# Kernel optimization log

Measured on AMD Instinct MI355X. Metric: run time of the kernel, lower is better.

Reference implementation:

```python
import jax, jax.numpy as jnp
import numpy as np

NUM_HEADS = 16


def _rel_shift(x):
    # x: [b, n, i, L]  (Transformer-XL relative shift trick)
    b, n, i, L = x.shape
    xt = jnp.transpose(x, (2, 3, 0, 1))              # [i, L, b, n]
    zero = jnp.zeros((i, 1, b, n), xt.dtype)
    xp = jnp.concatenate([zero, xt], axis=1)         # [i, L+1, b, n]
    xp = xp.reshape(L + 1, i, b, n)
    xt = xp[1:].reshape(i, L, b, n)
    return jnp.transpose(xt, (2, 3, 0, 1))


def _forward(x, bias, pos_emb, pos_bias_u, pos_bias_v, cache, indice_bool,
             sent_weights, Wq, bq, Wk, bk, Wv, bv, Wo, bo, Wr, br):
    B, I, H = x.shape
    nh = NUM_HEADS
    D = H // nh
    aff = lambda t, W, b: t @ W.T + b
    sh = lambda t: jnp.transpose(t.reshape(B, -1, nh, D), (0, 2, 1, 3))

    q, k, v = aff(x, Wq, bq), aff(x, Wk, bk), aff(x, Wv, bv)
    r = aff(jnp.swapaxes(pos_emb, 0, 1), Wr, br)
    qh, kh, vh, rh = sh(q), sh(k), sh(v), sh(r)

    N, cB, L, _ = cache.shape
    clen = N * L
    cflat = jnp.swapaxes(cache, 0, 1).reshape(cB, clen, H)
    ckh = jnp.transpose(sh(aff(cflat, Wk, bk)).reshape(cB, nh, N, L, D), (2, 0, 1, 3, 4))  # [N,B,nh,L,D]
    cvh = jnp.transpose(sh(aff(cflat, Wv, bv)).reshape(cB, nh, N, L, D), (2, 0, 1, 3, 4))
    cache_rh = jnp.transpose(rh[:, :, :clen].reshape(B, nh, N, L, D), (2, 0, 1, 3, 4))
    rh = rh[:, :, clen:]

    qh = qh * D ** -0.5
    quh = qh + pos_bias_u[:, None, :]
    qvh = qh + pos_bias_v[:, None, :]

    AC = jnp.einsum('bnid,bnjd->bnij', quh, kh) + bias
    BD = jnp.einsum('bnid,bnjd->bnij', qvh, rh)

    pre_AC = jnp.einsum('bnid,ibk->kbnid', quh, indice_bool)
    cAC = jnp.einsum('kbnid,kbnld->kbnil', pre_AC, ckh)
    cAC = jnp.transpose(cAC, (1, 2, 3, 0, 4)).reshape(B, nh, I, clen)
    AC = jnp.concatenate([cAC, AC], axis=-1)

    pre_BD = jnp.einsum('bnid,ibk->kbnid', qvh, indice_bool)
    cBD = jnp.einsum('kbnid,kbnld->kbnil', pre_BD, cache_rh)
    cBD = jnp.transpose(cBD, (1, 2, 3, 0, 4)).reshape(B, nh, I, clen)
    BD = jnp.concatenate([cBD, BD], axis=-1)

    logits = AC + _rel_shift(BD)
    w = jax.nn.softmax(logits, axis=-1)
    cw, w = w[..., :clen], w[..., clen:]

    cw = jnp.transpose(cw.reshape(B, nh, I, N, L), (3, 0, 1, 2, 4))  # [N,b,nh,i,L]
    cw = jnp.einsum('kbnij,ibk->bnikj', cw, sent_weights).reshape(B, nh, I, clen)
    cvh2 = jnp.transpose(cvh, (1, 2, 0, 3, 4)).reshape(B, nh, clen, D)

    out = (jnp.einsum('bnij,bnjd->bnid', w, vh)
           + jnp.einsum('bnij,bnjd->bnid', cw, cvh2))
    out = jnp.transpose(out, (0, 2, 1, 3)).reshape(B, I, H)
    return aff(out, Wo, bo)


def setup_inputs() -> dict:
    key = jax.random.key(0)
    ks = jax.random.split(key, 12)
    B, I, H, N, L = 4, 512, 1024, 4, 512
    R = N * L + I
    D = H // NUM_HEADS
    s = H ** -0.5
    return {
        'x': jax.random.normal(ks[0], (B, I, H), jnp.float32),
        'bias': jnp.zeros((1, 1, I, I), jnp.float32),
        'pos_emb': jax.random.normal(ks[1], (R, B, H), jnp.float32),
        'pos_bias_u': jax.random.normal(ks[2], (NUM_HEADS, D), jnp.float32),
        'pos_bias_v': jax.random.normal(ks[3], (NUM_HEADS, D), jnp.float32),
        'cache': jax.random.normal(ks[4], (N, B, L, H), jnp.float32),
        'indice_bool': jnp.ones((I, B, N), jnp.float32),
        'sent_weights': jax.random.uniform(ks[5], (I, B, N), jnp.float32),
        'Wq': jax.random.normal(ks[6], (H, H), jnp.float32) * s,
        'bq': jnp.zeros((H,), jnp.float32),
        'Wk': jax.random.normal(ks[7], (H, H), jnp.float32) * s,
        'bk': jnp.zeros((H,), jnp.float32),
        'Wv': jax.random.normal(ks[8], (H, H), jnp.float32) * s,
        'bv': jnp.zeros((H,), jnp.float32),
        'Wo': jax.random.normal(ks[9], (H, H), jnp.float32) * s,
        'bo': jnp.zeros((H,), jnp.float32),
        'Wr': jax.random.normal(ks[10], (H, H), jnp.float32) * s,
        'br': jnp.zeros((H,), jnp.float32),
    }


def reference(x, bias, pos_emb, pos_bias_u, pos_bias_v, cache, indice_bool,
              sent_weights, Wq, bq, Wk, bk, Wv, bv, Wo, bo, Wr, br):
    return _forward(x, bias, pos_emb, pos_bias_u, pos_bias_v, cache,
                    indice_bool, sent_weights, Wq, bq, Wk, bk, Wv, bv,
                    Wo, bo, Wr, br)
```

## Files before the change

kernel.cpp:

```cpp
#include <hip/hip_runtime.h>
#include <hip/hip_bf16.h>


typedef __hip_bfloat16 hbf16;
typedef __attribute__((ext_vector_type(8))) short short8;
typedef __attribute__((ext_vector_type(4))) short short4v;
typedef __attribute__((ext_vector_type(4))) float f32x4;

typedef __attribute__((address_space(1))) const unsigned int as1c_uint;
typedef __attribute__((address_space(3))) unsigned int as3_uint;

#define DEV static __device__ __forceinline__

DEV void gl_lds16(const void* g, void* l) {
  __builtin_amdgcn_global_load_lds((as1c_uint*)g, (as3_uint*)l, 16, 0, 0);
}

DEV short bf_bits(float f) {
  hbf16 h = __float2bfloat16(f);
  return __builtin_bit_cast(short, h);
}

DEV f32x4 mfma16(short8 a, short8 b, f32x4 c) {
  return __builtin_amdgcn_mfma_f32_16x16x32_bf16(a, b, c, 0, 0, 0);
}

__global__ __launch_bounds__(256) void pack_all(
    const float* __restrict__ x, const float* __restrict__ cache,
    const float* __restrict__ pe, const float* __restrict__ Wq,
    const float* __restrict__ Wk, const float* __restrict__ Wv,
    const float* __restrict__ Wo, const float* __restrict__ Wr,
    short* __restrict__ x_bf, short* __restrict__ cf_bf,
    short* __restrict__ pe_bf, short* __restrict__ wq_bf,
    short* __restrict__ wk_bf, short* __restrict__ wv_bf,
    short* __restrict__ wo_bf, short* __restrict__ wr_bf) {
  const int bid = blockIdx.x, tid = threadIdx.x;
  const float* src;
  short* dst;
  size_t sidx, didx;
  if (bid < 2048) {
    int c = bid * 256 + tid;
    src = x; dst = x_bf; sidx = c; didx = c;
  } else if (bid < 10240) {
    int c = (bid - 2048) * 256 + tid;
    int h4 = c & 255, m = c >> 8;
    int b = m >> 11, j = m & 2047;
    size_t srow = ((size_t)(j >> 9) * 4 + b) * 512 + (j & 511);
    src = cache; dst = cf_bf; sidx = srow * 256 + h4; didx = c;
  } else if (bid < 20480) {
    int c = (bid - 10240) * 256 + tid;
    int h4 = c & 255, m = c >> 8;
    int b = m / 2560, j = m - b * 2560;
    size_t srow = (size_t)j * 4 + b;
    src = pe; dst = pe_bf; sidx = srow * 256 + h4; didx = c;
  } else {
    int e = bid - 20480;
    int w = e >> 10;
    int c = (e & 1023) * 256 + tid;
    switch (w) {
      case 0: src = Wq; dst = wq_bf; break;
      case 1: src = Wk; dst = wk_bf; break;
      case 2: src = Wv; dst = wv_bf; break;
      case 3: src = Wo; dst = wo_bf; break;
      default: src = Wr; dst = wr_bf; break;
    }
    sidx = c; didx = c;
  }
  float4 v = ((const float4*)src)[sidx];
  short4v s; s.x = bf_bits(v.x); s.y = bf_bits(v.y); s.z = bf_bits(v.z); s.w = bf_bits(v.w);
  ((short4v*)dst)[didx] = s;
}

#define GEMM_KLOOP(Asrc, Wsrc)                                                  \
  f32x4 acc[4][4];                                                              \
  _Pragma("unroll") for (int a_ = 0; a_ < 4; a_++)                              \
  _Pragma("unroll") for (int b_ = 0; b_ < 4; b_++)                              \
      acc[a_][b_] = (f32x4){0.f, 0.f, 0.f, 0.f};                                \
  for (int k0 = 0; k0 < 1024; k0 += 32) {                                       \
    _Pragma("unroll") for (int q = 0; q < 2; q++) {                             \
      const int ci = (wid * 2 + q) * 64 + lane;                                 \
      const int r = ci >> 2, cc = (ci & 3) << 3;                                \
      gl_lds16(Asrc + (size_t)(m0 + r) * 1024 + k0 + cc,                        \
               (char*)As + (wid * 2 + q) * 1024);                               \
      gl_lds16(Wsrc + (size_t)(n0 + r) * 1024 + k0 + cc,                        \
               (char*)Bs + (wid * 2 + q) * 1024);                               \
    }                                                                           \
    __syncthreads();                                                            \
    short8 af[4], bfv[4];                                                       \
    _Pragma("unroll") for (int mi = 0; mi < 4; mi++)                            \
        af[mi] = *(const short8*)(As + (wm * 64 + mi * 16 + lr) * 32 + lk * 8); \
    _Pragma("unroll") for (int ni = 0; ni < 4; ni++)                            \
        bfv[ni] = *(const short8*)(Bs + (wn * 64 + ni * 16 + lr) * 32 + lk * 8);\
    _Pragma("unroll") for (int mi = 0; mi < 4; mi++)                            \
    _Pragma("unroll") for (int ni = 0; ni < 4; ni++)                            \
        acc[mi][ni] = mfma16(af[mi], bfv[ni], acc[mi][ni]);                     \
    __syncthreads();                                                            \
  }

__global__ __launch_bounds__(256) void gemm_kv(
    const short* __restrict__ A, const short* __restrict__ W,
    const float* __restrict__ bk, const float* __restrict__ bv,
    short* __restrict__ KF, short* __restrict__ VT) {
  __shared__ short As[128 * 32], Bs[128 * 32];
  const int tid = threadIdx.x, wid = tid >> 6, lane = tid & 63;
  const int lr = lane & 15, lk = lane >> 4;
  const int wm = wid >> 1, wn = wid & 1;
  const int flat = blockIdx.y * 16 + blockIdx.x;
  const int xcd = flat & 7, kk = flat >> 3;
  const int nt = kk & 15, mt = xcd * 10 + (kk >> 4);
  const int m0 = mt * 128, n0 = nt * 128;

  GEMM_KLOOP(A, W)

#pragma unroll
  for (int mi = 0; mi < 4; mi++) {
    const int mrow = m0 + wm * 64 + mi * 16 + lk * 4;
#pragma unroll
    for (int ni = 0; ni < 4; ni++) {
      const int col = n0 + wn * 64 + ni * 16 + lr;
      const float bc = (col < 1024) ? bk[col] : bv[col - 1024];
#pragma unroll
      for (int r = 0; r < 4; r++) {
        const int m = mrow + r;
        const float v = acc[mi][ni][r] + bc;
        int bb, jj;
        if (m < 8192) { bb = m >> 11; jj = m & 2047; }
        else { int mm = m - 8192; bb = mm >> 9; jj = 2048 + (mm & 511); }
        if (col < 1024) {
          const int n = col >> 6, d = col & 63;
          KF[((size_t)(bb * 16 + n) * 2560 + jj) * 64 + d] = bf_bits(v);
        } else {
          const int cv = col - 1024, n = cv >> 6, d = cv & 63;
          VT[((size_t)(bb * 16 + n) * 64 + d) * 2560 + jj] = bf_bits(v);
        }
      }
    }
  }
}

__global__ __launch_bounds__(256) void gemm_qr(
    const short* __restrict__ pe_bf, const short* __restrict__ x_bf,
    const short* __restrict__ Wr, const short* __restrict__ Wq,
    const float* __restrict__ br, const float* __restrict__ bq,
    const float* __restrict__ pu, const float* __restrict__ pv,
    short* __restrict__ RF, short* __restrict__ QU, short* __restrict__ QV) {
  __shared__ short As[128 * 32], Bs[128 * 32];
  const int tid = threadIdx.x, wid = tid >> 6, lane = tid & 63;
  const int lr = lane & 15, lk = lane >> 4;
  const int wm = wid >> 1, wn = wid & 1;
  const int flat = blockIdx.y * 8 + blockIdx.x;
  const int xcd = flat & 7, kk = flat >> 3;
  const int nt = kk & 7, mt = xcd * 12 + (kk >> 3);
  const bool isQ = (mt >= 80);
  const short* Asrc = isQ ? x_bf : pe_bf;
  const short* Wsrc = isQ ? Wq : Wr;
  const int m0 = (isQ ? mt - 80 : mt) * 128, n0 = nt * 128;

  GEMM_KLOOP(Asrc, Wsrc)

#pragma unroll
  for (int mi = 0; mi < 4; mi++) {
    const int mrow = m0 + wm * 64 + mi * 16 + lk * 4;
#pragma unroll
    for (int ni = 0; ni < 4; ni++) {
      const int col = n0 + wn * 64 + ni * 16 + lr;
      const float bc = isQ ? bq[col] : br[col];
      const int n = col >> 6, d = col & 63;
#pragma unroll
      for (int r = 0; r < 4; r++) {
        const int m = mrow + r;
        const float v = acc[mi][ni][r] + bc;
        if (isQ) {
          const int b = m >> 9, i = m & 511;
          const float qs = v * 0.125f;
          const size_t o = ((size_t)(b * 16 + n) * 512 + i) * 64 + d;
          QU[o] = bf_bits(qs + pu[col]);
          QV[o] = bf_bits(qs + pv[col]);
        } else {
          const int b = m / 2560, j = m - b * 2560;
          RF[((size_t)(b * 16 + n) * 2560 + j) * 64 + d] = bf_bits(v);
        }
      }
    }
  }
}

__global__ __launch_bounds__(256) void gemm_out(
    const short* __restrict__ A, const short* __restrict__ W,
    const float* __restrict__ bias, float* __restrict__ of) {
  __shared__ short As[128 * 32], Bs[128 * 32];
  const int tid = threadIdx.x, wid = tid >> 6, lane = tid & 63;
  const int lr = lane & 15, lk = lane >> 4;
  const int wm = wid >> 1, wn = wid & 1;
  const int flat = blockIdx.y * 8 + blockIdx.x;
  const int xcd = flat & 7, kk = flat >> 3;
  const int nt = kk & 7, mt = xcd * 2 + (kk >> 3);
  const int m0 = mt * 128, n0 = nt * 128;

  GEMM_KLOOP(A, W)

#pragma unroll
  for (int mi = 0; mi < 4; mi++) {
    const int mrow = m0 + wm * 64 + mi * 16 + lk * 4;
#pragma unroll
    for (int ni = 0; ni < 4; ni++) {
      const int col = n0 + wn * 64 + ni * 16 + lr;
      const float bc = bias[col];
#pragma unroll
      for (int r = 0; r < 4; r++)
        of[(size_t)(mrow + r) * 1024 + col] = acc[mi][ni][r] + bc;
    }
  }
}

__global__ __launch_bounds__(256, 2) void fused_attn(
    const short* __restrict__ QU, const short* __restrict__ QV,
    const short* __restrict__ KF, const short* __restrict__ RF,
    const short* __restrict__ VT, const float* __restrict__ ib,
    const float* __restrict__ sw, const float* __restrict__ bias,
    short* __restrict__ attn) {
  __shared__ short Ks[2][64 * 64];
  __shared__ short Rs[2][128 * 64];
  __shared__ float PsU[4][16 * 84];
  __shared__ float ibs[65 * 4];
  __shared__ float sws[64 * 4];

  const int tid = threadIdx.x, wid = tid >> 6, lane = tid & 63;
  const int p = blockIdx.x, it = blockIdx.y;
  const int b = p >> 4, hn = p & 15;
  const int I0 = it * 64, iw = wid * 16;
  const int lr = lane & 15, lg4 = lane >> 4;
  float* Psw = PsU[wid];
  short* Ptw = (short*)Psw;

  for (int t5 = tid; t5 < 260; t5 += 256) {
    int r = t5 >> 2, k = t5 & 3;
    int gi = I0 + r; if (gi > 511) gi = 511;
    ibs[t5] = ib[gi * 16 + b * 4 + k];
  }
  {
    int r = tid >> 2, k = tid & 3;
    sws[tid] = sw[(I0 + r) * 16 + b * 4 + k];
  }

  short8 qu[2], qv[2], qvp[2];
  {
    const short* QUb = QU + ((size_t)p * 512 + I0) * 64;
    const short* QVb = QV + ((size_t)p * 512 + I0) * 64;
    int rowp = I0 + iw + lr + 1; if (rowp > 511) rowp = 511;
    const short* QVn = QV + ((size_t)p * 512 + rowp) * 64;
#pragma unroll
    for (int s = 0; s < 2; s++) {
      qu[s]  = *(const short8*)(QUb + (iw + lr) * 64 + s * 32 + lg4 * 8);
      qv[s]  = *(const short8*)(QVb + (iw + lr) * 64 + s * 32 + lg4 * 8);
      qvp[s] = *(const short8*)(QVn + s * 32 + lg4 * 8);
    }
  }
  const short* KFp = KF + (size_t)p * 2560 * 64;
  const short* RFp = RF + (size_t)p * 2560 * 64;
  const short* VTp = VT + (size_t)p * 64 * 2560;

  auto stageK = [&](int j0, int buf) {
#pragma unroll
    for (int q = 0; q < 2; q++) {
      int e = wid * 2 + q;
      int row = e * 8 + (lane >> 3);
      int ch = (lane & 7) ^ (row & 7);
      gl_lds16(KFp + (size_t)(j0 + row) * 64 + ch * 8,
               (char*)Ks + buf * 8192 + e * 1024);
    }
  };
  auto stageR = [&](int band, int buf) {
#pragma unroll
    for (int q = 0; q < 4; q++) {
      int e = wid * 4 + q;
      int row = e * 8 + (lane >> 3);
      int rg = band + row; rg = rg < 0 ? 0 : (rg > 2559 ? 2559 : rg);
      int ch = (lane & 7) ^ (row & 7);
      gl_lds16(RFp + (size_t)rg * 64 + ch * 8,
               (char*)Rs + buf * 16384 + e * 1024);
    }
  };
  auto bfragK = [&](int buf, int row, int s) -> short8 {
    return *(const short8*)((const char*)Ks + buf * 8192 + row * 128 +
                            (((s * 4 + lg4) ^ (row & 7)) << 4));
  };
  auto bfragR = [&](int buf, int row, int s) -> short8 {
    return *(const short8*)((const char*)Rs + buf * 16384 + row * 128 +
                            (((s * 4 + lg4) ^ (row & 7)) << 4));
  };
  auto bd_lds = [&](short8 a0, short8 a1, int ro, int band, int buf) {
#pragma unroll
    for (int ctl = 0; ctl < 5; ctl++) {
      int cidx = (3 - wid) * 16 + ctl * 16 + lr;
      f32x4 acc = (f32x4){0.f, 0.f, 0.f, 0.f};
      acc = mfma16(a0, bfragR(buf, cidx, 0), acc);
      acc = mfma16(a1, bfragR(buf, cidx, 1), acc);
      int scol = band + cidx;
#pragma unroll
      for (int r = 0; r < 4; r++) {
        int ii = lg4 * 4 + r;
        float v = acc[r];
        if ((unsigned)scol < 2048u) v *= ibs[(iw + ii + ro) * 4 + (scol >> 9)];
        Psw[ii * 84 + ctl * 16 + lr] = v;
      }
    }
  };
  auto bd_glb = [&](short8 a0, short8 a1, int ro, int band) {
#pragma unroll
    for (int ctl = 0; ctl < 5; ctl++) {
      int cidx = (3 - wid) * 16 + ctl * 16 + lr;
      int rg = band + cidx; rg = rg < 0 ? 0 : (rg > 2559 ? 2559 : rg);
      const short* rb = RFp + (size_t)rg * 64 + lg4 * 8;
      short8 b0 = *(const short8*)(rb);
      short8 b1 = *(const short8*)(rb + 32);
      f32x4 acc = (f32x4){0.f, 0.f, 0.f, 0.f};
      acc = mfma16(a0, b0, acc);
      acc = mfma16(a1, b1, acc);
      int scol = band + cidx;
#pragma unroll
      for (int r = 0; r < 4; r++) {
        int ii = lg4 * 4 + r;
        float v = acc[r];
        if ((unsigned)scol < 2048u) v *= ibs[(iw + ii + ro) * 4 + (scol >> 9)];
        Psw[ii * 84 + ctl * 16 + lr] = v;
      }
    }
  };

  float m_[4], l_[4];
  f32x4 o[4];
#pragma unroll
  for (int r = 0; r < 4; r++) { m_[r] = -1e30f; l_[r] = 0.f; }
#pragma unroll
  for (int dt = 0; dt < 4; dt++) o[dt] = (f32x4){0.f, 0.f, 0.f, 0.f};

  {
    const int tb0 = 448 - I0;
    stageK(0, 0);
    stageR((tb0 <= 2559) ? tb0 : tb0 - 2561, 0);
  }
  __syncthreads();
  int cur = 0;

  for (int j0 = 0; j0 < 2560; j0 += 64) {
    const int tb = j0 + 448 - I0;
    const bool ph1 = (tb <= 2559);
    const bool strad = ph1 && (tb >= 2435);

    if (j0 + 64 < 2560) {
      const int tbn = tb + 64;
      stageK(j0 + 64, cur ^ 1);
      stageR((tbn <= 2559) ? tbn : tbn - 2561, cur ^ 1);
    }

    short8 vf0[4], vf1[4];
#pragma unroll
    for (int q = 0; q < 4; q++) {
      const short* vb = VTp + (size_t)(q * 16 + lr) * 2560 + j0 + lg4 * 8;
      vf0[q] = *(const short8*)(vb);
      vf1[q] = *(const short8*)(vb + 32);
    }

    f32x4 lgt[4];
#pragma unroll
    for (int jt = 0; jt < 4; jt++) {
      f32x4 acc = (f32x4){0.f, 0.f, 0.f, 0.f};
      acc = mfma16(qu[0], bfragK(cur, jt * 16 + lr, 0), acc);
      acc = mfma16(qu[1], bfragK(cur, jt * 16 + lr, 1), acc);
      lgt[jt] = acc;
    }
    if (j0 < 2048) {
      float s0[4];
#pragma unroll
      for (int r = 0; r < 4; r++) s0[r] = ibs[(iw + lg4 * 4 + r) * 4 + (j0 >> 9)];
#pragma unroll
      for (int jt = 0; jt < 4; jt++)
#pragma unroll
        for (int r = 0; r < 4; r++) lgt[jt][r] *= s0[r];
    } else {
#pragma unroll
      for (int jt = 0; jt < 4; jt++)
#pragma unroll
        for (int r = 0; r < 4; r++) {
          int i = I0 + iw + lg4 * 4 + r;
          lgt[jt][r] += bias[(size_t)i * 512 + (j0 - 2048) + jt * 16 + lr];
        }
    }

    if (ph1) bd_lds(qv[0], qv[1], 0, tb, cur);
    else     bd_lds(qvp[0], qvp[1], 1, tb - 2561, cur);
#pragma unroll
    for (int jt = 0; jt < 4; jt++)
#pragma unroll
      for (int r = 0; r < 4; r++) {
        int ii = lg4 * 4 + r;
        int jl = jt * 16 + lr;
        int t = tb + 63 + jl - (iw + ii);
        bool ok = ph1 ? (t <= 2559) : (t >= 2561);
        if (ok) lgt[jt][r] += Psw[ii * 83 + 15 + jl];
      }
    if (strad) {
      bd_glb(qvp[0], qvp[1], 1, tb - 2561);
#pragma unroll
      for (int jt = 0; jt < 4; jt++)
#pragma unroll
        for (int r = 0; r < 4; r++) {
          int ii = lg4 * 4 + r;
          int jl = jt * 16 + lr;
          int t = tb + 63 + jl - (iw + ii);
          if (t >= 2561) lgt[jt][r] += Psw[ii * 83 + 15 + jl];
        }
    }

    float pm[4];
#pragma unroll
    for (int r = 0; r < 4; r++) {
      float v = fmaxf(fmaxf(lgt[0][r], lgt[1][r]), fmaxf(lgt[2][r], lgt[3][r]));
      v = fmaxf(v, __shfl_xor(v, 1));
      v = fmaxf(v, __shfl_xor(v, 2));
      v = fmaxf(v, __shfl_xor(v, 4));
      v = fmaxf(v, __shfl_xor(v, 8));
      pm[r] = v;
    }
    const bool grow = (pm[0] > m_[0]) | (pm[1] > m_[1]) | (pm[2] > m_[2]) | (pm[3] > m_[3]);
    if (__any(grow)) {
#pragma unroll
      for (int r = 0; r < 4; r++) {
        float rm = fmaxf(m_[r], pm[r]);
        float sc = __expf(m_[r] - rm);
        m_[r] = rm;
        l_[r] *= sc;
#pragma unroll
        for (int dt = 0; dt < 4; dt++) o[dt][r] *= sc;
      }
    }
    float swv[4];
#pragma unroll
    for (int r = 0; r < 4; r++)
      swv[r] = (j0 < 2048) ? sws[(iw + lg4 * 4 + r) * 4 + (j0 >> 9)] : 1.f;
    float rs[4] = {0.f, 0.f, 0.f, 0.f};
#pragma unroll
    for (int jt = 0; jt < 4; jt++)
#pragma unroll
      for (int r = 0; r < 4; r++) {
        float pe_ = __expf(lgt[jt][r] - m_[r]);
        rs[r] += pe_;
        Ptw[(lg4 * 4 + r) * 72 + jt * 16 + lr] = bf_bits(pe_ * swv[r]);
      }
#pragma unroll
    for (int r = 0; r < 4; r++) {
      float v = rs[r];
      v += __shfl_xor(v, 1);
      v += __shfl_xor(v, 2);
      v += __shfl_xor(v, 4);
      v += __shfl_xor(v, 8);
      l_[r] += v;
    }

    short8 pa0 = *(const short8*)((const char*)Ptw + lr * 144 + lg4 * 16);
    short8 pa1 = *(const short8*)((const char*)Ptw + lr * 144 + 64 + lg4 * 16);
#pragma unroll
    for (int dt = 0; dt < 4; dt++) {
      o[dt] = mfma16(pa0, vf0[dt], o[dt]);
      o[dt] = mfma16(pa1, vf1[dt], o[dt]);
    }

    __syncthreads();
    cur ^= 1;
  }

#pragma unroll
  for (int dt = 0; dt < 4; dt++)
#pragma unroll
    for (int r = 0; r < 4; r++) {
      int i = I0 + iw + lg4 * 4 + r;
      int d = dt * 16 + lr;
      attn[((size_t)(b * 512 + i)) * 1024 + hn * 64 + d] = bf_bits(o[dt][r] / l_[r]);
    }
}


extern "C" void kernel_launch(void* const* d_in, const int* in_sizes, int n_in,
                              void* d_out, int out_size, void* d_ws, size_t ws_size,
                              hipStream_t stream) {
  (void)in_sizes; (void)n_in; (void)out_size; (void)ws_size;
  const float* x    = (const float*)d_in[0];
  const float* bias = (const float*)d_in[1];
  const float* pe   = (const float*)d_in[2];
  const float* pu   = (const float*)d_in[3];
  const float* pv   = (const float*)d_in[4];
  const float* cache= (const float*)d_in[5];
  const float* ib   = (const float*)d_in[6];
  const float* sw   = (const float*)d_in[7];
  const float* Wq   = (const float*)d_in[8];
  const float* bq   = (const float*)d_in[9];
  const float* Wk   = (const float*)d_in[10];
  const float* bk   = (const float*)d_in[11];
  const float* Wv   = (const float*)d_in[12];
  const float* bv   = (const float*)d_in[13];
  const float* Wo   = (const float*)d_in[14];
  const float* bo   = (const float*)d_in[15];
  const float* Wr   = (const float*)d_in[16];
  const float* br   = (const float*)d_in[17];
  float* out = (float*)d_out;

  char* ws = (char*)d_ws;
  size_t off = 0;
  auto alloc = [&](size_t bytes) -> char* {
    char* ptr = ws + off;
    off = (off + bytes + 255) & ~(size_t)255;
    return ptr;
  };
  short* cf_bf = (short*)alloc((size_t)8192 * 1024 * 2);
  short* x_bf  = (short*)alloc((size_t)2048 * 1024 * 2);
  short* pe_bf = (short*)alloc((size_t)10240 * 1024 * 2);
  short* wk_bf = (short*)alloc((size_t)1024 * 1024 * 2);
  short* wv_bf = (short*)alloc((size_t)1024 * 1024 * 2);
  short* wq_bf = (short*)alloc((size_t)1024 * 1024 * 2);
  short* wo_bf = (short*)alloc((size_t)1024 * 1024 * 2);
  short* wr_bf = (short*)alloc((size_t)1024 * 1024 * 2);
  short* QU    = (short*)alloc((size_t)64 * 512 * 64 * 2);
  short* QV    = (short*)alloc((size_t)64 * 512 * 64 * 2);
  short* KF    = (short*)alloc((size_t)64 * 2560 * 64 * 2);
  short* RF    = (short*)alloc((size_t)64 * 2560 * 64 * 2);
  short* VT    = (short*)alloc((size_t)64 * 2560 * 64 * 2);
  short* attn  = (short*)alloc((size_t)2048 * 1024 * 2);

  pack_all<<<25600, 256, 0, stream>>>(x, cache, pe, Wq, Wk, Wv, Wo, Wr,
                                      x_bf, cf_bf, pe_bf, wq_bf, wk_bf,
                                      wv_bf, wo_bf, wr_bf);

  gemm_qr<<<dim3(8, 96), 256, 0, stream>>>(pe_bf, x_bf, wr_bf, wq_bf, br, bq,
                                           pu, pv, RF, QU, QV);
  gemm_kv<<<dim3(16, 80), 256, 0, stream>>>(cf_bf, wk_bf, bk, bv, KF, VT);

  fused_attn<<<dim3(64, 8), 256, 0, stream>>>(QU, QV, KF, RF, VT, ib, sw, bias, attn);

  gemm_out<<<dim3(8, 16), 256, 0, stream>>>(attn, wo_bf, bo, out);
}
```

Before: 359.0 us.

## Split attention key range in two with flash-decoding combine kernel

The fused attention kernel now splits the 2560-long key range into two halves across blockIdx.y, doubling the grid. Each half writes unnormalized partial outputs plus running max and sum to fp32 workspace, and a new combine kernel merges them into bf16 attention output. The R tile is no longer staged in LDS; BD fragments are read straight from global memory, which shrinks LDS so launch bounds can ask for 4 blocks per SIMD set. The trade is extra global traffic for the partial buffers, uncached R loads, and one more kernel launch, in exchange for more parallelism and occupancy.

```diff
diff --git a/kernel.cpp b/kernel.cpp
--- a/kernel.cpp
+++ b/kernel.cpp
@@ -213,21 +213,22 @@
   }
 }
 
-__global__ __launch_bounds__(256, 2) void fused_attn(
+__global__ __launch_bounds__(256, 4) void fused_attn(
     const short* __restrict__ QU, const short* __restrict__ QV,
     const short* __restrict__ KF, const short* __restrict__ RF,
     const short* __restrict__ VT, const float* __restrict__ ib,
     const float* __restrict__ sw, const float* __restrict__ bias,
-    short* __restrict__ attn) {
+    float* __restrict__ Po, float* __restrict__ Pm, float* __restrict__ Pl) {
   __shared__ short Ks[2][64 * 64];
-  __shared__ short Rs[2][128 * 64];
   __shared__ float PsU[4][16 * 84];
   __shared__ float ibs[65 * 4];
   __shared__ float sws[64 * 4];
 
   const int tid = threadIdx.x, wid = tid >> 6, lane = tid & 63;
-  const int p = blockIdx.x, it = blockIdx.y;
-  const int b = p >> 4, hn = p & 15;
+  const int p = blockIdx.x;
+  const int yy = blockIdx.y;
+  const int split = yy >> 3, it = yy & 7;
+  const int b = p >> 4;
   const int I0 = it * 64, iw = wid * 16;
   const int lr = lane & 15, lg4 = lane >> 4;
   float* Psw = PsU[wid];
@@ -270,43 +271,11 @@
                (char*)Ks + buf * 8192 + e * 1024);
     }
   };
-  auto stageR = [&](int band, int buf) {
-#pragma unroll
-    for (int q = 0; q < 4; q++) {
-      int e = wid * 4 + q;
-      int row = e * 8 + (lane >> 3);
-      int rg = band + row; rg = rg < 0 ? 0 : (rg > 2559 ? 2559 : rg);
-      int ch = (lane & 7) ^ (row & 7);
-      gl_lds16(RFp + (size_t)rg * 64 + ch * 8,
-               (char*)Rs + buf * 16384 + e * 1024);
-    }
-  };
   auto bfragK = [&](int buf, int row, int s) -> short8 {
     return *(const short8*)((const char*)Ks + buf * 8192 + row * 128 +
                             (((s * 4 + lg4) ^ (row & 7)) << 4));
   };
-  auto bfragR = [&](int buf, int row, int s) -> short8 {
-    return *(const short8*)((const char*)Rs + buf * 16384 + row * 128 +
-                            (((s * 4 + lg4) ^ (row & 7)) << 4));
-  };
-  auto bd_lds = [&](short8 a0, short8 a1, int ro, int band, int buf) {
-#pragma unroll
-    for (int ctl = 0; ctl < 5; ctl++) {
-      int cidx = (3 - wid) * 16 + ctl * 16 + lr;
-      f32x4 acc = (f32x4){0.f, 0.f, 0.f, 0.f};
-      acc = mfma16(a0, bfragR(buf, cidx, 0), acc);
-      acc = mfma16(a1, bfragR(buf, cidx, 1), acc);
-      int scol = band + cidx;
-#pragma unroll
-      for (int r = 0; r < 4; r++) {
-        int ii = lg4 * 4 + r;
-        float v = acc[r];
-        if ((unsigned)scol < 2048u) v *= ibs[(iw + ii + ro) * 4 + (scol >> 9)];
-        Psw[ii * 84 + ctl * 16 + lr] = v;
-      }
-    }
-  };
-  auto bd_glb = [&](short8 a0, short8 a1, int ro, int band) {
+  auto bd_pass = [&](short8 a0, short8 a1, int ro, int band) {
 #pragma unroll
     for (int ctl = 0; ctl < 5; ctl++) {
       int cidx = (3 - wid) * 16 + ctl * 16 + lr;
@@ -335,24 +304,17 @@
 #pragma unroll
   for (int dt = 0; dt < 4; dt++) o[dt] = (f32x4){0.f, 0.f, 0.f, 0.f};
 
-  {
-    const int tb0 = 448 - I0;
-    stageK(0, 0);
-    stageR((tb0 <= 2559) ? tb0 : tb0 - 2561, 0);
-  }
+  const int j0beg = split * 1280, j0end = j0beg + 1280;
+  stageK(j0beg, 0);
   __syncthreads();
   int cur = 0;
 
-  for (int j0 = 0; j0 < 2560; j0 += 64) {
+  for (int j0 = j0beg; j0 < j0end; j0 += 64) {
     const int tb = j0 + 448 - I0;
     const bool ph1 = (tb <= 2559);
     const bool strad = ph1 && (tb >= 2435);
 
-    if (j0 + 64 < 2560) {
-      const int tbn = tb + 64;
-      stageK(j0 + 64, cur ^ 1);
-      stageR((tbn <= 2559) ? tbn : tbn - 2561, cur ^ 1);
-    }
+    if (j0 + 64 < j0end) stageK(j0 + 64, cur ^ 1);
 
     short8 vf0[4], vf1[4];
 #pragma unroll
@@ -388,8 +350,8 @@
         }
     }
 
-    if (ph1) bd_lds(qv[0], qv[1], 0, tb, cur);
-    else     bd_lds(qvp[0], qvp[1], 1, tb - 2561, cur);
+    if (ph1) bd_pass(qv[0], qv[1], 0, tb);
+    else     bd_pass(qvp[0], qvp[1], 1, tb - 2561);
 #pragma unroll
     for (int jt = 0; jt < 4; jt++)
 #pragma unroll
@@ -401,7 +363,7 @@
         if (ok) lgt[jt][r] += Psw[ii * 83 + 15 + jl];
       }
     if (strad) {
-      bd_glb(qvp[0], qvp[1], 1, tb - 2561);
+      bd_pass(qvp[0], qvp[1], 1, tb - 2561);
 #pragma unroll
       for (int jt = 0; jt < 4; jt++)
 #pragma unroll
@@ -470,14 +432,46 @@
     cur ^= 1;
   }
 
+  const size_t SPL = (size_t)64 * 512 * 64;
+  float* Pob = Po + (size_t)split * SPL + ((size_t)p * 512 + I0 + iw) * 64;
 #pragma unroll
   for (int dt = 0; dt < 4; dt++)
 #pragma unroll
+    for (int r = 0; r < 4; r++)
+      Pob[(size_t)(lg4 * 4 + r) * 64 + dt * 16 + lr] = o[dt][r];
+  if (lr == 0) {
+#pragma unroll
     for (int r = 0; r < 4; r++) {
-      int i = I0 + iw + lg4 * 4 + r;
-      int d = dt * 16 + lr;
-      attn[((size_t)(b * 512 + i)) * 1024 + hn * 64 + d] = bf_bits(o[dt][r] / l_[r]);
-    }
+      int idx = split * 32768 + p * 512 + I0 + iw + lg4 * 4 + r;
+      Pm[idx] = m_[r];
+      Pl[idx] = l_[r];
+    }
+  }
+}
+
+__global__ __launch_bounds__(256) void combine_k(const float* __restrict__ Po,
+                                                 const float* __restrict__ Pm,
+                                                 const float* __restrict__ Pl,
+                                                 short* __restrict__ attn) {
+  int idx = blockIdx.x * 256 + threadIdx.x;
+  int d4 = idx & 15, i = (idx >> 4) & 511, p = idx >> 13;
+  int b = p >> 4, hn = p & 15;
+  const size_t SPL = (size_t)64 * 512 * 64;
+  size_t base = ((size_t)p * 512 + i) * 64 + d4 * 4;
+  float4 o0 = *(const float4*)(Po + base);
+  float4 o1 = *(const float4*)(Po + SPL + base);
+  int mi = p * 512 + i;
+  float m0 = Pm[mi], m1 = Pm[32768 + mi];
+  float l0 = Pl[mi], l1 = Pl[32768 + mi];
+  float mm = fmaxf(m0, m1);
+  float s0 = __expf(m0 - mm), s1 = __expf(m1 - mm);
+  float inv = 1.f / (l0 * s0 + l1 * s1);
+  short4v r;
+  r.x = bf_bits((o0.x * s0 + o1.x * s1) * inv);
+  r.y = bf_bits((o0.y * s0 + o1.y * s1) * inv);
+  r.z = bf_bits((o0.z * s0 + o1.z * s1) * inv);
+  r.w = bf_bits((o0.w * s0 + o1.w * s1) * inv);
+  ((short4v*)(attn + ((size_t)(b * 512 + i) * 1024 + hn * 64)))[d4] = r;
 }
 
 
@@ -526,6 +520,9 @@
   short* RF    = (short*)alloc((size_t)64 * 2560 * 64 * 2);
   short* VT    = (short*)alloc((size_t)64 * 2560 * 64 * 2);
   short* attn  = (short*)alloc((size_t)2048 * 1024 * 2);
+  float* Po    = (float*)alloc((size_t)2 * 64 * 512 * 64 * 4);
+  float* Pm    = (float*)alloc((size_t)2 * 64 * 512 * 4);
+  float* Pl    = (float*)alloc((size_t)2 * 64 * 512 * 4);
 
   pack_all<<<25600, 256, 0, stream>>>(x, cache, pe, Wq, Wk, Wv, Wo, Wr,
                                       x_bf, cf_bf, pe_bf, wq_bf, wk_bf,
@@ -535,7 +532,9 @@
                                            pu, pv, RF, QU, QV);
   gemm_kv<<<dim3(16, 80), 256, 0, stream>>>(cf_bf, wk_bf, bk, bv, KF, VT);
 
-  fused_attn<<<dim3(64, 8), 256, 0, stream>>>(QU, QV, KF, RF, VT, ib, sw, bias, attn);
+  fused_attn<<<dim3(64, 16), 256, 0, stream>>>(QU, QV, KF, RF, VT, ib, sw,
+                                               bias, Po, Pm, Pl);
+  combine_k<<<2048, 256, 0, stream>>>(Po, Pm, Pl, attn);
 
   gemm_out<<<dim3(8, 16), 256, 0, stream>>>(attn, wo_bf, bo, out);
 }
```

New measurement: 491.3 us. +36.9%, slower.
